# Kernel optimization log

Hardware: AMD Instinct MI355X
Metric: run time of the kernel (lower is better)

Reference implementation:

```python
import jax, jax.numpy as jnp
import numpy as np

B, S, D, H = 8, 1024, 1024, 16
HD = D // H  # head_dim = 64
SCALE = HD ** -0.5


def setup_inputs() -> dict:
    key = jax.random.key(0)
    ks = jax.random.split(key, 10)
    std = D ** -0.5
    return {
        "hidden_states": jax.random.normal(ks[0], (B, S, D), jnp.float32),
        "attn_mask": jnp.zeros((B, 1, S, S), jnp.float32),
        "prev_attn_weights": jax.random.normal(ks[1], (B, H, S, S), jnp.float32),
        "Wq": jax.random.normal(ks[2], (D, D), jnp.float32) * std,
        "bq": jnp.zeros((D,), jnp.float32),
        "Wk": jax.random.normal(ks[3], (D, D), jnp.float32) * std,
        "bk": jnp.zeros((D,), jnp.float32),
        "Wv": jax.random.normal(ks[4], (D, D), jnp.float32) * std,
        "bv": jnp.zeros((D,), jnp.float32),
    }


def _split_heads(x):
    # (B, S, D) -> (B, H, S, HD)
    return x.reshape(B, S, H, HD).transpose(0, 2, 1, 3)


def reference(hidden_states, attn_mask, prev_attn_weights, Wq, bq, Wk, bk, Wv, bv):
    q = _split_heads(hidden_states @ Wq + bq)
    k = _split_heads(hidden_states @ Wk + bk)
    v = _split_heads(hidden_states @ Wv + bv)
    # scaled dot-product scores + additive mask + realformer residual scores
    scores = jnp.einsum("bhqd,bhkd->bhqk", q, k) * SCALE
    scores = scores + attn_mask + prev_attn_weights
    probs = jax.nn.softmax(scores, axis=-1)  # dropout p=0 (eval)
    ctx = jnp.einsum("bhqk,bhkd->bhqd", probs, v)
    # (B, H, S, HD) -> (B, S, D)
    out = ctx.transpose(0, 2, 1, 3).reshape(B, S, D)
    return out
```

## Files before the change

### kernel.cpp

```cpp
#include <hip/hip_runtime.h>

#define B_  8
#define S_  1024
#define D_  1024
#define H_  16
#define HD_ 64
#define M_  8192
#define LOG2E 1.44269504088896f
#define QSCALE_ (0.125f * 1.44269504088896f)
#define MSHIFT_ 20.0f

typedef __attribute__((ext_vector_type(8))) short bf16x8;
typedef __attribute__((ext_vector_type(4))) float f32x4;

__device__ __forceinline__ unsigned short f2b(float x) {
  union { float f; unsigned u; } un; un.f = x;
  unsigned r = un.u + 0x7FFFu + ((un.u >> 16) & 1u);
  return (unsigned short)(r >> 16);
}

__global__ __launch_bounds__(256) void k_convert_x(const float* __restrict__ x,
                                                   unsigned short* __restrict__ o) {
  int i = (blockIdx.x * 256 + threadIdx.x) * 4;
  const int n = M_ * D_;
  const int stride = gridDim.x * 256 * 4;
  for (; i < n; i += stride) {
    const float4 v = *(const float4*)(x + i);
    ushort4 r;
    r.x = f2b(v.x); r.y = f2b(v.y); r.z = f2b(v.z); r.w = f2b(v.w);
    *(ushort4*)(o + i) = r;
  }
}

__global__ __launch_bounds__(256) void k_transpose_w(const float* __restrict__ Wq,
    const float* __restrict__ Wk, const float* __restrict__ Wv,
    unsigned short* __restrict__ Wt) {
  __shared__ float t[64][65];
  const float* W = (blockIdx.z == 0) ? Wq : ((blockIdx.z == 1) ? Wk : Wv);
  unsigned short* dst = Wt + (size_t)blockIdx.z * (D_ * D_);
  const int k0 = blockIdx.x * 64, n0 = blockIdx.y * 64;
  const int tid = threadIdx.x;
#pragma unroll
  for (int i = 0; i < 16; ++i) {
    const int lin = i * 256 + tid;
    const int r = lin >> 6, c = lin & 63;
    t[r][c] = W[(size_t)(k0 + r) * D_ + n0 + c];
  }
  __syncthreads();
#pragma unroll
  for (int i = 0; i < 16; ++i) {
    const int lin = i * 256 + tid;
    const int r = lin >> 6, c = lin & 63;
    dst[(size_t)(n0 + r) * D_ + k0 + c] = f2b(t[c][r]);
  }
}

__global__ __launch_bounds__(256) void k_proj(const unsigned short* __restrict__ X,
    const unsigned short* __restrict__ Wt,
    const float* __restrict__ bq, const float* __restrict__ bk, const float* __restrict__ bv,
    unsigned short* __restrict__ Qw, unsigned short* __restrict__ Kw,
    unsigned short* __restrict__ Vt) {
  __shared__ unsigned short xs[128 * 32];
  __shared__ unsigned short wsh[128 * 32];
  const int tid = threadIdx.x;
  const int lane = tid & 63, wv = tid >> 6;
  const int g = lane >> 4, li = lane & 15;
  const int m0 = blockIdx.x * 128;
  const int mode = (blockIdx.y >= 16);
  const int n0 = (mode ? (blockIdx.y - 16) : blockIdx.y) * 128;
  const int wr = wv >> 1, wc = wv & 1;
  const int wtrow0 = mode ? (2048 + n0) : n0;

  f32x4 acc[4][4];
#pragma unroll
  for (int i = 0; i < 4; ++i)
#pragma unroll
    for (int j = 0; j < 4; ++j) acc[i][j] = (f32x4){0.f, 0.f, 0.f, 0.f};

  const int srow = wv * 32 + (lane >> 2);
  const int skel = (lane & 3) * 8;

  for (int k0 = 0; k0 < D_; k0 += 32) {
#pragma unroll
    for (int i = 0; i < 2; ++i) {
      const unsigned short* gx = X + (size_t)(m0 + srow + i * 16) * D_ + k0 + skel;
      const unsigned short* gw = Wt + (size_t)(wtrow0 + srow + i * 16) * D_ + k0 + skel;
      __builtin_amdgcn_global_load_lds(
          (const __attribute__((address_space(1))) void*)gx,
          (__attribute__((address_space(3))) void*)&xs[(wv * 32 + i * 16) * 32], 16, 0, 0);
      __builtin_amdgcn_global_load_lds(
          (const __attribute__((address_space(1))) void*)gw,
          (__attribute__((address_space(3))) void*)&wsh[(wv * 32 + i * 16) * 32], 16, 0, 0);
    }
    __syncthreads();
    bf16x8 af[4], bfr[4];
#pragma unroll
    for (int i = 0; i < 4; ++i) {
      const int ar = wr * 64 + i * 16 + li;
      const int br = wc * 64 + i * 16 + li;
      if (!mode) {
        af[i]  = *(const bf16x8*)&xs[ar * 32 + g * 8];
        bfr[i] = *(const bf16x8*)&wsh[br * 32 + g * 8];
      } else {
        af[i]  = *(const bf16x8*)&wsh[ar * 32 + g * 8];
        bfr[i] = *(const bf16x8*)&xs[br * 32 + g * 8];
      }
    }
#pragma unroll
    for (int i = 0; i < 4; ++i)
#pragma unroll
      for (int j = 0; j < 4; ++j)
        acc[i][j] = __builtin_amdgcn_mfma_f32_16x16x32_bf16(af[i], bfr[j], acc[i][j], 0, 0, 0);
    __syncthreads();
  }

  if (!mode) {
#pragma unroll
    for (int j = 0; j < 4; ++j) {
      const int n = n0 + wc * 64 + j * 16 + li;
      const float bias = (n < D_) ? bq[n] : bk[n - D_];
#pragma unroll
      for (int i = 0; i < 4; ++i) {
#pragma unroll
        for (int r = 0; r < 4; ++r) {
          const int m = m0 + wr * 64 + i * 16 + g * 4 + r;
          const float v = acc[i][j][r] + bias;
          const int bb = m >> 10, ss = m & 1023;
          if (n < D_) {
            Qw[((size_t)(bb * H_ + (n >> 6)) * S_ + ss) * HD_ + (n & 63)] = f2b(v * QSCALE_);
          } else {
            const int nk = n - D_;
            Kw[((size_t)(bb * H_ + (nk >> 6)) * S_ + ss) * HD_ + (nk & 63)] = f2b(v);
          }
        }
      }
    }
  } else {
#pragma unroll
    for (int i = 0; i < 4; ++i) {
#pragma unroll
      for (int r = 0; r < 4; ++r) {
        const int nv = n0 + wr * 64 + i * 16 + g * 4 + r;
        const float bias = bv[nv];
#pragma unroll
        for (int j = 0; j < 4; ++j) {
          const int m = m0 + wc * 64 + j * 16 + li;
          const int bb = m >> 10, ss = m & 1023;
          const float v = acc[i][j][r] + bias;
          Vt[((size_t)(bb * H_ + (nv >> 6)) * HD_ + (nv & 63)) * S_ + ss] = f2b(v);
        }
      }
    }
  }
}

__global__ __launch_bounds__(256, 2) void k_attn(const unsigned short* __restrict__ Qw,
    const unsigned short* __restrict__ Kw, const unsigned short* __restrict__ Vt,
    const float* __restrict__ prev, const float* __restrict__ mask,
    float* __restrict__ out) {
  __shared__ unsigned short k_s[2][4096];
  __shared__ unsigned short v_s[2][4096];
  __shared__ float pm_s[2][4][1024];
  __shared__ unsigned short p_lds[4][16][72];
  const int tid = threadIdx.x;
  const int lane = tid & 63, wv = tid >> 6;
  const int g = lane >> 4, li = lane & 15;

  const int phys = blockIdx.x + 16 * blockIdx.y;
  const int xcd = phys & 7, idx = phys >> 3;
  const int qt = idx & 15;
  const int bh = xcd + 8 * (idx >> 4);
  const int b = bh >> 4, h = bh & 15;
  const int q0 = qt * 64 + wv * 16;

  const unsigned short* kbase = Kw + (size_t)bh * S_ * HD_;
  const unsigned short* vbase = Vt + (size_t)bh * HD_ * S_;
  const float* pbase = prev + (size_t)bh * S_ * S_ + (size_t)q0 * S_;
  const float* mb    = mask + (size_t)b * S_ * S_ + (size_t)(q0 + li) * S_ + g * 4;

  bf16x8 qf[2];
  {
    const unsigned short* qp = Qw + ((size_t)bh * S_ + q0 + li) * HD_ + g * 8;
    qf[0] = *(const bf16x8*)qp;
    qf[1] = *(const bf16x8*)(qp + 32);
  }

  const int rloc8 = lane >> 3;
  const int csw8  = (((lane & 7) ^ rloc8) << 3);
  const int prow4 = lane >> 4;
  const int pchnk = lane & 15;

#define STAGE(TN, BI)                                                                      \
  {                                                                                        \
    const int sn = (TN) * 64;                                                              \
    _Pragma("unroll")                                                                      \
    for (int i = 0; i < 2; ++i) {                                                          \
      const int row = wv * 16 + i * 8 + rloc8;                                             \
      __builtin_amdgcn_global_load_lds(                                                    \
          (const __attribute__((address_space(1))) void*)(kbase + (size_t)(sn + row) * HD_ + csw8), \
          (__attribute__((address_space(3))) void*)(&k_s[BI][0] + (wv * 16 + i * 8) * 64), 16, 0, 0); \
      __builtin_amdgcn_global_load_lds(                                                    \
          (const __attribute__((address_space(1))) void*)(vbase + (size_t)row * S_ + sn + csw8), \
          (__attribute__((address_space(3))) void*)(&v_s[BI][0] + (wv * 16 + i * 8) * 64), 16, 0, 0); \
    }                                                                                      \
    _Pragma("unroll")                                                                      \
    for (int i = 0; i < 4; ++i) {                                                          \
      const int row = i * 4 + prow4;                                                       \
      __builtin_amdgcn_global_load_lds(                                                    \
          (const __attribute__((address_space(1))) void*)(pbase + (size_t)row * S_ + sn + ((pchnk ^ (row & 7)) << 2)), \
          (__attribute__((address_space(3))) void*)(&pm_s[BI][wv][i * 256]), 16, 0, 0);    \
    }                                                                                      \
  }

  float lrun = 0.f;
  f32x4 ctx[4];
#pragma unroll
  for (int d = 0; d < 4; ++d) ctx[d] = (f32x4){0.f, 0.f, 0.f, 0.f};

  f32x4 mA[4], mB[4];

  STAGE(0, 0);
#pragma unroll
  for (int cb = 0; cb < 4; ++cb) mA[cb] = *(const f32x4*)(mb + cb * 16);

#define PHASE(T, PB, NB, MCUR, MNXT)                                                  \
  {                                                                                   \
    const int tn = ((T) < 15) ? (T) + 1 : 15;                                         \
    STAGE(tn, NB);                                                                    \
    _Pragma("unroll")                                                                 \
    for (int cb = 0; cb < 4; ++cb)                                                    \
      MNXT[cb] = *(const f32x4*)(mb + tn * 64 + cb * 16);                             \
    asm volatile("s_waitcnt vmcnt(12)" ::: "memory");                                 \
    __builtin_amdgcn_s_barrier();                                                     \
    {                                                                                 \
      const unsigned short* kb = &k_s[PB][0];                                         \
      const unsigned short* vb = &v_s[PB][0];                                         \
      const float* pmw = &pm_s[PB][wv][0];                                            \
      f32x4 sa[4];                                                                    \
      _Pragma("unroll")                                                               \
      for (int cb = 0; cb < 4; ++cb) {                                                \
        const int r = cb * 16 + li;                                                   \
        const bf16x8 k0 = *(const bf16x8*)(kb + r * 64 + ((g ^ (li & 7)) << 3));      \
        const bf16x8 k1 = *(const bf16x8*)(kb + r * 64 + (((4 + g) ^ (li & 7)) << 3)); \
        f32x4 z = (f32x4){0.f, 0.f, 0.f, 0.f};                                        \
        z      = __builtin_amdgcn_mfma_f32_16x16x32_bf16(k0, qf[0], z, 0, 0, 0);      \
        sa[cb] = __builtin_amdgcn_mfma_f32_16x16x32_bf16(k1, qf[1], z, 0, 0, 0);      \
      }                                                                               \
      _Pragma("unroll")                                                               \
      for (int cb = 0; cb < 4; ++cb) {                                                \
        const f32x4 pv = *(const f32x4*)(pmw + li * 64 + (((cb * 4 + g) ^ (li & 7)) << 2)); \
        f32x4 pmc;                                                                    \
        pmc.x = fmaf(pv.x + MCUR[cb].x, LOG2E, -MSHIFT_);                             \
        pmc.y = fmaf(pv.y + MCUR[cb].y, LOG2E, -MSHIFT_);                             \
        pmc.z = fmaf(pv.z + MCUR[cb].z, LOG2E, -MSHIFT_);                             \
        pmc.w = fmaf(pv.w + MCUR[cb].w, LOG2E, -MSHIFT_);                             \
        const float e0 = exp2f(sa[cb][0] + pmc.x);                                    \
        const float e1 = exp2f(sa[cb][1] + pmc.y);                                    \
        const float e2 = exp2f(sa[cb][2] + pmc.z);                                    \
        const float e3 = exp2f(sa[cb][3] + pmc.w);                                    \
        lrun += (e0 + e1) + (e2 + e3);                                                \
        ushort4 pw;                                                                   \
        pw.x = f2b(e0); pw.y = f2b(e1); pw.z = f2b(e2); pw.w = f2b(e3);               \
        *(ushort4*)&p_lds[wv][li][cb * 16 + g * 4] = pw;                              \
      }                                                                               \
      bf16x8 pf0 = *(const bf16x8*)&p_lds[wv][li][g * 8];                             \
      bf16x8 pf1 = *(const bf16x8*)&p_lds[wv][li][32 + g * 8];                        \
      _Pragma("unroll")                                                               \
      for (int d = 0; d < 4; ++d) {                                                   \
        const int r = d * 16 + li;                                                    \
        const bf16x8 v0 = *(const bf16x8*)(vb + r * 64 + ((g ^ (li & 7)) << 3));      \
        const bf16x8 v1 = *(const bf16x8*)(vb + r * 64 + (((4 + g) ^ (li & 7)) << 3)); \
        ctx[d] = __builtin_amdgcn_mfma_f32_16x16x32_bf16(pf0, v0, ctx[d], 0, 0, 0);   \
        ctx[d] = __builtin_amdgcn_mfma_f32_16x16x32_bf16(pf1, v1, ctx[d], 0, 0, 0);   \
      }                                                                               \
    }                                                                                 \
    __builtin_amdgcn_s_barrier();                                                     \
  }

  for (int t = 0; t < 16; t += 2) {
    PHASE(t,     0, 1, mA, mB);
    PHASE(t + 1, 1, 0, mB, mA);
  }
#undef PHASE
#undef STAGE

  asm volatile("s_waitcnt vmcnt(0)" ::: "memory");

  lrun += __shfl_xor(lrun, 16);
  lrun += __shfl_xor(lrun, 32);
#pragma unroll
  for (int j = 0; j < 4; ++j) {
    const float rs = __shfl(lrun, g * 4 + j);
    const float inv = 1.0f / rs;
    const int q = q0 + g * 4 + j;
    float* op = out + ((size_t)b * S_ + q) * D_ + h * HD_ + li;
#pragma unroll
    for (int d = 0; d < 4; ++d)
      op[d * 16] = ctx[d][j] * inv;
  }
}

extern "C" void kernel_launch(void* const* d_in, const int* in_sizes, int n_in,
                              void* d_out, int out_size, void* d_ws, size_t ws_size,
                              hipStream_t stream) {
  const float* hs   = (const float*)d_in[0];
  const float* mask = (const float*)d_in[1];
  const float* prev = (const float*)d_in[2];
  const float* Wq   = (const float*)d_in[3];
  const float* bq   = (const float*)d_in[4];
  const float* Wk   = (const float*)d_in[5];
  const float* bk   = (const float*)d_in[6];
  const float* Wv   = (const float*)d_in[7];
  const float* bv   = (const float*)d_in[8];
  float* out = (float*)d_out;

  char* ws = (char*)d_ws;
  unsigned short* Xbf = (unsigned short*)ws;
  unsigned short* Wt  = (unsigned short*)(ws + (16ull << 20));
  unsigned short* Qw  = (unsigned short*)(ws + (22ull << 20));
  unsigned short* Kw  = (unsigned short*)(ws + (38ull << 20));
  unsigned short* Vt  = (unsigned short*)(ws + (54ull << 20));

  k_convert_x<<<2048, 256, 0, stream>>>(hs, Xbf);
  k_transpose_w<<<dim3(16, 16, 3), 256, 0, stream>>>(Wq, Wk, Wv, Wt);
  k_proj<<<dim3(64, 24), 256, 0, stream>>>(Xbf, Wt, bq, bk, bv, Qw, Kw, Vt);
  k_attn<<<dim3(16, 128), 256, 0, stream>>>(Qw, Kw, Vt, prev, mask, out);
}
```

Measured before the change: 267.8 us.

## Store mask as bf16, group batches per XCD, stream prev with nontemporal hint

A new pre-pass converts the additive attention mask to bf16, and the attention kernel reads it as ushort4, expanding each value back to fp32 before the softmax arithmetic. This halves the mask bytes the attention kernel reads. The block-to-(batch, head, q-tile) mapping is changed so that every block of one batch runs on the same XCD, so that batch's mask can be reused from that XCD's L2 across heads. The prev_attn_weights loads into LDS now carry a cache-policy hint meant to stream them past the cache instead of evicting reused data. In exchange, it adds an extra kernel launch plus a full read and write pass over the mask, and mask values lose precision when rounded to bf16.

```diff
diff --git a/kernel.cpp b/kernel.cpp
--- a/kernel.cpp
+++ b/kernel.cpp
@@ -18,11 +18,27 @@
   unsigned r = un.u + 0x7FFFu + ((un.u >> 16) & 1u);
   return (unsigned short)(r >> 16);
 }
+__device__ __forceinline__ float b2f(unsigned short s) {
+  union { unsigned u; float f; } c; c.u = ((unsigned)s) << 16; return c.f;
+}
 
 __global__ __launch_bounds__(256) void k_convert_x(const float* __restrict__ x,
                                                    unsigned short* __restrict__ o) {
   int i = (blockIdx.x * 256 + threadIdx.x) * 4;
   const int n = M_ * D_;
+  const int stride = gridDim.x * 256 * 4;
+  for (; i < n; i += stride) {
+    const float4 v = *(const float4*)(x + i);
+    ushort4 r;
+    r.x = f2b(v.x); r.y = f2b(v.y); r.z = f2b(v.z); r.w = f2b(v.w);
+    *(ushort4*)(o + i) = r;
+  }
+}
+
+__global__ __launch_bounds__(256) void k_convert_mask(const float* __restrict__ x,
+                                                      unsigned short* __restrict__ o) {
+  int i = (blockIdx.x * 256 + threadIdx.x) * 4;
+  const int n = B_ * S_ * S_;
   const int stride = gridDim.x * 256 * 4;
   for (; i < n; i += stride) {
     const float4 v = *(const float4*)(x + i);
@@ -156,7 +172,7 @@
 
 __global__ __launch_bounds__(256, 2) void k_attn(const unsigned short* __restrict__ Qw,
     const unsigned short* __restrict__ Kw, const unsigned short* __restrict__ Vt,
-    const float* __restrict__ prev, const float* __restrict__ mask,
+    const float* __restrict__ prev, const unsigned short* __restrict__ Mb,
     float* __restrict__ out) {
   __shared__ unsigned short k_s[2][4096];
   __shared__ unsigned short v_s[2][4096];
@@ -167,16 +183,17 @@
   const int g = lane >> 4, li = lane & 15;
 
   const int phys = blockIdx.x + 16 * blockIdx.y;
-  const int xcd = phys & 7, idx = phys >> 3;
-  const int qt = idx & 15;
-  const int bh = xcd + 8 * (idx >> 4);
-  const int b = bh >> 4, h = bh & 15;
+  const int b  = phys & 7;
+  const int j  = phys >> 3;
+  const int h  = (j & 7) + 8 * ((j >> 7) & 1);
+  const int qt = (j >> 3) & 15;
+  const int bh = b * H_ + h;
   const int q0 = qt * 64 + wv * 16;
 
   const unsigned short* kbase = Kw + (size_t)bh * S_ * HD_;
   const unsigned short* vbase = Vt + (size_t)bh * HD_ * S_;
   const float* pbase = prev + (size_t)bh * S_ * S_ + (size_t)q0 * S_;
-  const float* mb    = mask + (size_t)b * S_ * S_ + (size_t)(q0 + li) * S_ + g * 4;
+  const unsigned short* mb = Mb + (size_t)b * S_ * S_ + (size_t)(q0 + li) * S_ + g * 4;
 
   bf16x8 qf[2];
   {
@@ -208,7 +225,7 @@
       const int row = i * 4 + prow4;                                                       \
       __builtin_amdgcn_global_load_lds(                                                    \
           (const __attribute__((address_space(1))) void*)(pbase + (size_t)row * S_ + sn + ((pchnk ^ (row & 7)) << 2)), \
-          (__attribute__((address_space(3))) void*)(&pm_s[BI][wv][i * 256]), 16, 0, 0);    \
+          (__attribute__((address_space(3))) void*)(&pm_s[BI][wv][i * 256]), 16, 0, 2);    \
     }                                                                                      \
   }
 
@@ -217,11 +234,11 @@
 #pragma unroll
   for (int d = 0; d < 4; ++d) ctx[d] = (f32x4){0.f, 0.f, 0.f, 0.f};
 
-  f32x4 mA[4], mB[4];
+  ushort4 mA[4], mB4[4];
 
   STAGE(0, 0);
 #pragma unroll
-  for (int cb = 0; cb < 4; ++cb) mA[cb] = *(const f32x4*)(mb + cb * 16);
+  for (int cb = 0; cb < 4; ++cb) mA[cb] = *(const ushort4*)(mb + cb * 16);
 
 #define PHASE(T, PB, NB, MCUR, MNXT)                                                  \
   {                                                                                   \
@@ -229,7 +246,7 @@
     STAGE(tn, NB);                                                                    \
     _Pragma("unroll")                                                                 \
     for (int cb = 0; cb < 4; ++cb)                                                    \
-      MNXT[cb] = *(const f32x4*)(mb + tn * 64 + cb * 16);                             \
+      MNXT[cb] = *(const ushort4*)(mb + tn * 64 + cb * 16);                           \
     asm volatile("s_waitcnt vmcnt(12)" ::: "memory");                                 \
     __builtin_amdgcn_s_barrier();                                                     \
     {                                                                                 \
@@ -249,11 +266,12 @@
       _Pragma("unroll")                                                               \
       for (int cb = 0; cb < 4; ++cb) {                                                \
         const f32x4 pv = *(const f32x4*)(pmw + li * 64 + (((cb * 4 + g) ^ (li & 7)) << 2)); \
+        const ushort4 mu = MCUR[cb];                                                  \
         f32x4 pmc;                                                                    \
-        pmc.x = fmaf(pv.x + MCUR[cb].x, LOG2E, -MSHIFT_);                             \
-        pmc.y = fmaf(pv.y + MCUR[cb].y, LOG2E, -MSHIFT_);                             \
-        pmc.z = fmaf(pv.z + MCUR[cb].z, LOG2E, -MSHIFT_);                             \
-        pmc.w = fmaf(pv.w + MCUR[cb].w, LOG2E, -MSHIFT_);                             \
+        pmc.x = fmaf(pv.x + b2f(mu.x), LOG2E, -MSHIFT_);                              \
+        pmc.y = fmaf(pv.y + b2f(mu.y), LOG2E, -MSHIFT_);                              \
+        pmc.z = fmaf(pv.z + b2f(mu.z), LOG2E, -MSHIFT_);                              \
+        pmc.w = fmaf(pv.w + b2f(mu.w), LOG2E, -MSHIFT_);                              \
         const float e0 = exp2f(sa[cb][0] + pmc.x);                                    \
         const float e1 = exp2f(sa[cb][1] + pmc.y);                                    \
         const float e2 = exp2f(sa[cb][2] + pmc.z);                                    \
@@ -278,8 +296,8 @@
   }
 
   for (int t = 0; t < 16; t += 2) {
-    PHASE(t,     0, 1, mA, mB);
-    PHASE(t + 1, 1, 0, mB, mA);
+    PHASE(t,     0, 1, mA, mB4);
+    PHASE(t + 1, 1, 0, mB4, mA);
   }
 #undef PHASE
 #undef STAGE
@@ -289,14 +307,14 @@
   lrun += __shfl_xor(lrun, 16);
   lrun += __shfl_xor(lrun, 32);
 #pragma unroll
-  for (int j = 0; j < 4; ++j) {
-    const float rs = __shfl(lrun, g * 4 + j);
+  for (int j2 = 0; j2 < 4; ++j2) {
+    const float rs = __shfl(lrun, g * 4 + j2);
     const float inv = 1.0f / rs;
-    const int q = q0 + g * 4 + j;
+    const int q = q0 + g * 4 + j2;
     float* op = out + ((size_t)b * S_ + q) * D_ + h * HD_ + li;
 #pragma unroll
     for (int d = 0; d < 4; ++d)
-      op[d * 16] = ctx[d][j] * inv;
+      op[d * 16] = ctx[d][j2] * inv;
   }
 }
 
@@ -320,9 +338,11 @@
   unsigned short* Qw  = (unsigned short*)(ws + (22ull << 20));
   unsigned short* Kw  = (unsigned short*)(ws + (38ull << 20));
   unsigned short* Vt  = (unsigned short*)(ws + (54ull << 20));
+  unsigned short* Mbf = (unsigned short*)(ws + (70ull << 20));
 
   k_convert_x<<<2048, 256, 0, stream>>>(hs, Xbf);
+  k_convert_mask<<<2048, 256, 0, stream>>>(mask, Mbf);
   k_transpose_w<<<dim3(16, 16, 3), 256, 0, stream>>>(Wq, Wk, Wv, Wt);
   k_proj<<<dim3(64, 24), 256, 0, stream>>>(Xbf, Wt, bq, bk, bv, Qw, Kw, Vt);
-  k_attn<<<dim3(16, 128), 256, 0, stream>>>(Qw, Kw, Vt, prev, mask, out);
-}
+  k_attn<<<dim3(16, 128), 256, 0, stream>>>(Qw, Kw, Vt, prev, Mbf, out);
+}
```

New measurement: 282.8 us. 5.6% more time.
